# Optimization experiments

Measured on AMD Instinct MI355X. Metric: run time of the kernel, lower is better.

Reference implementation:

```python
import jax, jax.numpy as jnp
import numpy as np

N = 512
CZ = 128
CI = 128
LN_EPS = 1e-5


def _ln(x, w, b):
    m = jnp.mean(x, axis=-1, keepdims=True)
    v = jnp.mean(jnp.square(x - m), axis=-1, keepdims=True)
    return (x - m) * jax.lax.rsqrt(v + LN_EPS) * w + b


def setup_inputs() -> dict:
    key = jax.random.key(0)
    ks = jax.random.split(key, 8)
    s = 0.02
    return {
        "act": jax.random.normal(ks[0], (N, N, CZ), jnp.float32),
        "mask": jnp.ones((N, N), jnp.float32),
        "ln_in_w": jnp.ones((CZ,), jnp.float32),
        "ln_in_b": jnp.zeros((CZ,), jnp.float32),
        "proj_w": jax.random.normal(ks[1], (2 * CI, CZ), jnp.float32) * s,
        "proj_b": jnp.zeros((2 * CI,), jnp.float32),
        "gate_w": jax.random.normal(ks[2], (2 * CI, CI), jnp.float32) * s,
        "gate_b": jnp.zeros((2 * CI,), jnp.float32),
        "cn_w": jnp.ones((CI,), jnp.float32),
        "cn_b": jnp.zeros((CI,), jnp.float32),
        "outp_w": jax.random.normal(ks[3], (CZ, CI), jnp.float32) * s,
        "outp_b": jnp.zeros((CZ,), jnp.float32),
        "gl_w": jax.random.normal(ks[4], (CZ, CZ), jnp.float32) * s,
        "gl_b": jnp.zeros((CZ,), jnp.float32),
    }


def reference(act, mask, ln_in_w, ln_in_b, proj_w, proj_b, gate_w, gate_b,
              cn_w, cn_b, outp_w, outp_b, gl_w, gl_b):
    m = mask[..., None]                                    # [N,N,1]
    left = _ln(act, ln_in_w, ln_in_b)                      # [N,N,cz]
    proj = m * (left @ proj_w.T + proj_b)                  # [N,N,2ci]
    proj = proj * jax.nn.sigmoid(left @ gate_w.T + gate_b)
    ci = proj.shape[-1] // 2
    left_proj, right_proj = proj[..., :ci], proj[..., ci:]
    # triangle multiplication 'ikc,jkc->ijc' (outgoing edges)
    out = jnp.einsum('ikc,jkc->ijc', left_proj, right_proj)
    out = _ln(out, cn_w, cn_b)
    out = out @ outp_w.T + outp_b                          # [N,N,cz]
    out = out * jax.nn.sigmoid(left @ gl_w.T + gl_b)
    return out
```

## Files before the change

### kernel.cpp

```cpp
#include <hip/hip_runtime.h>
#include <stdint.h>

typedef unsigned short u16;
typedef uint32_t u32;
typedef _Float16 f16x8 __attribute__((ext_vector_type(8)));
typedef u16 u16x8 __attribute__((ext_vector_type(8)));
typedef float f32x4 __attribute__((ext_vector_type(4)));

#define MFMA(a,b,c) __builtin_amdgcn_mfma_f32_16x16x32_f16((a),(b),(c),0,0,0)

constexpr int SN = 512;
constexpr int CC = 128;
constexpr int PP = SN * SN;
constexpr float LNEPS = 1e-5f;
constexpr float LO_SCALE = 2048.0f;
constexpr float LO_INV   = 1.0f / 2048.0f;

__device__ __forceinline__ float bq(float f){
    u32 u = __builtin_bit_cast(u32, f);
    u += 0x7fffu + ((u >> 16) & 1u);
    return __builtin_bit_cast(float, u & 0xffff0000u);
}

__device__ __forceinline__ void split2(float x, u16& h, u16& l){
    _Float16 a = (_Float16)x;
    _Float16 b = (_Float16)((x - (float)a) * LO_SCALE);
    h = __builtin_bit_cast(u16, a);
    l = __builtin_bit_cast(u16, b);
}
__device__ __forceinline__ u16 f2h(float f){
    _Float16 h = (_Float16)f;
    return __builtin_bit_cast(u16, h);
}
__device__ __forceinline__ f16x8 ld_frag(const u16* p){
    return __builtin_bit_cast(f16x8, *(const u16x8*)p);
}
__device__ __forceinline__ float sigm(float x){ return 1.0f / (1.0f + __expf(-x)); }

__device__ __forceinline__ void load_w64s(const float* __restrict__ src,
                                          u16* dh, u16* dl, int tid){
    const int r = tid >> 2, q = tid & 3;
    const float4* s4 = (const float4*)(src + (size_t)r * CC + q * 32);
    __align__(16) u16 hbuf[32], lbuf[32];
    #pragma unroll
    for (int j = 0; j < 8; ++j){
        float4 v = s4[j];
        split2(bq(v.x), hbuf[j*4+0], lbuf[j*4+0]);
        split2(bq(v.y), hbuf[j*4+1], lbuf[j*4+1]);
        split2(bq(v.z), hbuf[j*4+2], lbuf[j*4+2]);
        split2(bq(v.w), hbuf[j*4+3], lbuf[j*4+3]);
    }
    uint4* ph = (uint4*)(dh + r * 136 + q * 32);
    uint4* pl = (uint4*)(dl + r * 136 + q * 32);
    #pragma unroll
    for (int w = 0; w < 4; ++w){
        ph[w] = ((const uint4*)hbuf)[w];
        pl[w] = ((const uint4*)lbuf)[w];
    }
}

__device__ __forceinline__ void ln_split(const float* __restrict__ act, int p0,
        const float* __restrict__ lnw, const float* __restrict__ lnb,
        u16* sLh, u16* sLl, int tid){
    const int pos = tid >> 2, q = tid & 3;
    const float4* a4 = (const float4*)(act + (size_t)(p0 + pos) * CC + q * 32);
    float4 av[8];
    float s = 0.f, s2 = 0.f;
    #pragma unroll
    for (int j = 0; j < 8; ++j){
        av[j] = a4[j];
        av[j].x = bq(av[j].x); av[j].y = bq(av[j].y);
        av[j].z = bq(av[j].z); av[j].w = bq(av[j].w);
        s  += av[j].x + av[j].y + av[j].z + av[j].w;
        s2 += av[j].x*av[j].x + av[j].y*av[j].y + av[j].z*av[j].z + av[j].w*av[j].w;
    }
    s  += __shfl_xor(s, 1);  s  += __shfl_xor(s, 2);
    s2 += __shfl_xor(s2, 1); s2 += __shfl_xor(s2, 2);
    const float mean = s * (1.f / CC);
    const float rstd = rsqrtf(s2 * (1.f / CC) - mean * mean + LNEPS);
    const float4* w4 = (const float4*)(lnw + q * 32);
    const float4* b4 = (const float4*)(lnb + q * 32);
    __align__(16) u16 hbuf[32], lbuf[32];
    #pragma unroll
    for (int j = 0; j < 8; ++j){
        float4 w = w4[j], b = b4[j];
        split2((av[j].x - mean) * rstd * bq(w.x) + bq(b.x), hbuf[j*4+0], lbuf[j*4+0]);
        split2((av[j].y - mean) * rstd * bq(w.y) + bq(b.y), hbuf[j*4+1], lbuf[j*4+1]);
        split2((av[j].z - mean) * rstd * bq(w.z) + bq(b.z), hbuf[j*4+2], lbuf[j*4+2]);
        split2((av[j].w - mean) * rstd * bq(w.w) + bq(b.w), hbuf[j*4+3], lbuf[j*4+3]);
    }
    uint4* ph = (uint4*)(sLh + pos * 136 + q * 32);
    uint4* pl = (uint4*)(sLl + pos * 136 + q * 32);
    #pragma unroll
    for (int w = 0; w < 4; ++w){
        ph[w] = ((const uint4*)hbuf)[w];
        pl[w] = ((const uint4*)lbuf)[w];
    }
}

__device__ __forceinline__ void gemm64s(const u16* sLh, const u16* sLl,
        const u16* sWh, const u16* sWl, int wave, int lq, int lr, f32x4* res){
    f32x4 ah[4], al[4];
    #pragma unroll
    for (int t = 0; t < 4; ++t){ ah[t] = f32x4{0,0,0,0}; al[t] = f32x4{0,0,0,0}; }
    #pragma unroll
    for (int kk = 0; kk < 4; ++kk){
        const int ao = (wave*16 + lr) * 136 + kk * 32 + lq * 8;
        const f16x8 a_h = ld_frag(sLh + ao);
        const f16x8 a_l = ld_frag(sLl + ao);
        #pragma unroll
        for (int t = 0; t < 4; ++t){
            const int bo = (t*16 + lr) * 136 + kk * 32 + lq * 8;
            const f16x8 b_h = ld_frag(sWh + bo);
            const f16x8 b_l = ld_frag(sWl + bo);
            ah[t] = MFMA(a_h, b_h, ah[t]);
            al[t] = MFMA(a_h, b_l, al[t]);
            al[t] = MFMA(a_l, b_h, al[t]);
        }
    }
    #pragma unroll
    for (int t = 0; t < 4; ++t) res[t] = ah[t] + al[t] * LO_INV;
}

__global__ __launch_bounds__(256) void k1_ln_proj(
        const float* __restrict__ act,  const float* __restrict__ mask,
        const float* __restrict__ lnw,  const float* __restrict__ lnb,
        const float* __restrict__ projw,const float* __restrict__ projb,
        const float* __restrict__ gatew,const float* __restrict__ gateb,
        u16* __restrict__ lph, u16* __restrict__ lpl,
        u16* __restrict__ rph, u16* __restrict__ rpl)
{
    __shared__ __align__(16) u16 sLh[64*136], sLl[64*136];
    __shared__ __align__(16) u16 sW[2*64*136];
    u16* sWh = sW;
    u16* sWl = sW + 64*136;

    const int tid  = threadIdx.x;
    const int p0   = blockIdx.x * 64;
    const int irow = p0 >> 9;
    const int k0   = p0 & 511;

    ln_split(act, p0, lnw, lnb, sLh, sLl, tid);

    const int wave = tid >> 6, lane = tid & 63, lq = lane >> 4, lr = lane & 15;
    const float4 mv = *(const float4*)(mask + p0 + wave*16 + lq*4);
    const float mr[4] = {bq(mv.x), bq(mv.y), bq(mv.z), bq(mv.w)};

    #pragma unroll 1
    for (int gh = 0; gh < 4; ++gh){
        const int g = gh >> 1, h = gh & 1;
        const int cb = g * 128 + h * 64;

        __syncthreads();
        load_w64s(gatew + (size_t)cb * CC, sWh, sWl, tid);
        __syncthreads();
        f32x4 gres[4]; gemm64s(sLh, sLl, sWh, sWl, wave, lq, lr, gres);
        __syncthreads();
        load_w64s(projw + (size_t)cb * CC, sWh, sWl, tid);
        __syncthreads();
        f32x4 pres[4]; gemm64s(sLh, sLl, sWh, sWl, wave, lq, lr, pres);
        __syncthreads();

        u16* sTh = sW;
        u16* sTl = sW + 64*72;
        const int pos0 = wave * 16 + lq * 4;
        #pragma unroll
        for (int t = 0; t < 4; ++t){
            const int col = t * 16 + lr;
            const float qb = bq(gateb[cb + col]);
            const float pb = bq(projb[cb + col]);
            __align__(8) u16 th[4], tl[4];
            #pragma unroll
            for (int r = 0; r < 4; ++r){
                const float v = mr[r] * (pres[t][r] + pb) * sigm(gres[t][r] + qb);
                split2(v, th[r], tl[r]);
            }
            *(uint2*)(sTh + col * 72 + pos0) = *(const uint2*)th;
            *(uint2*)(sTl + col * 72 + pos0) = *(const uint2*)tl;
        }
        __syncthreads();

        {
            const int cl = tid >> 2, q = tid & 3;
            const size_t off = (size_t)(h*64 + cl) * PP + (size_t)irow * SN + k0 + q * 16;
            u16* dh = (g ? rph : lph) + off;
            const u16* sh = sTh + cl * 72 + q * 16;
            ((uint4*)dh)[0] = ((const uint4*)sh)[0];
            ((uint4*)dh)[1] = ((const uint4*)sh)[1];
            u16* lob = g ? rpl : lpl;
            if (lob){
                u16* dl = lob + off;
                const u16* sl = sTl + cl * 72 + q * 16;
                ((uint4*)dl)[0] = ((const uint4*)sl)[0];
                ((uint4*)dl)[1] = ((const uint4*)sl)[1];
            }
        }
    }
}

template<int RPS, int OT16>
__global__ __launch_bounds__(256) void k2_einsum(
        const u16* __restrict__ lph, const u16* __restrict__ lpl,
        const u16* __restrict__ rph, const u16* __restrict__ rpl,
        void* __restrict__ outTv)
{
    __shared__ __align__(16) u16 sAh[128*72], sAl[128*72], sBh[128*72];
    __shared__ __align__(16) u16 sBl[RPS ? 128*72 : 8];
    const int tid = threadIdx.x;
    const int bid = blockIdx.x;
    const int swz = (bid & 7) * 256 + (bid >> 3);
    const int c   = swz >> 4;
    const int i0  = ((swz >> 2) & 3) * 128;
    const int j0  = (swz & 3) * 128;
    const size_t aoff = (size_t)c * PP + (size_t)i0 * SN;
    const size_t boff = (size_t)c * PP + (size_t)j0 * SN;
    const int wave = tid >> 6, lane = tid & 63, lq = lane >> 4, lr = lane & 15;
    const int wi = (wave & 1) * 64, wj = (wave >> 1) * 64;
    const int row = tid >> 1, half = tid & 1;
    const size_t goff = (size_t)row * SN + half * 32;

    f32x4 acch[4][4], accl[4][4];
    #pragma unroll
    for (int m = 0; m < 4; ++m)
        #pragma unroll
        for (int n = 0; n < 4; ++n){ acch[m][n] = f32x4{0,0,0,0}; accl[m][n] = f32x4{0,0,0,0}; }

    for (int k0 = 0; k0 < SN; k0 += 64){
        const uint4* gah = (const uint4*)(lph + aoff + goff + k0);
        const uint4* gal = (const uint4*)(lpl + aoff + goff + k0);
        const uint4* gbh = (const uint4*)(rph + boff + goff + k0);
        uint4 Ah0 = gah[0], Ah1 = gah[1], Ah2 = gah[2], Ah3 = gah[3];
        uint4 Al0 = gal[0], Al1 = gal[1], Al2 = gal[2], Al3 = gal[3];
        uint4 Bh0 = gbh[0], Bh1 = gbh[1], Bh2 = gbh[2], Bh3 = gbh[3];
        uint4 Bl0, Bl1, Bl2, Bl3;
        if (RPS){
            const uint4* gbl = (const uint4*)(rpl + boff + goff + k0);
            Bl0 = gbl[0]; Bl1 = gbl[1]; Bl2 = gbl[2]; Bl3 = gbl[3];
        }
        __syncthreads();
        uint4* dah = (uint4*)(sAh + row * 72 + half * 32);
        uint4* dal = (uint4*)(sAl + row * 72 + half * 32);
        uint4* dbh = (uint4*)(sBh + row * 72 + half * 32);
        dah[0] = Ah0; dah[1] = Ah1; dah[2] = Ah2; dah[3] = Ah3;
        dal[0] = Al0; dal[1] = Al1; dal[2] = Al2; dal[3] = Al3;
        dbh[0] = Bh0; dbh[1] = Bh1; dbh[2] = Bh2; dbh[3] = Bh3;
        if (RPS){
            uint4* dbl = (uint4*)(sBl + row * 72 + half * 32);
            dbl[0] = Bl0; dbl[1] = Bl1; dbl[2] = Bl2; dbl[3] = Bl3;
        }
        __syncthreads();
        #pragma unroll
        for (int kk = 0; kk < 64; kk += 32){
            f16x8 ahf[4], alf[4], bhf[4], blf[RPS ? 4 : 1];
            #pragma unroll
            for (int m = 0; m < 4; ++m){
                const int ro = (wi + m*16 + lr) * 72 + kk + lq * 8;
                ahf[m] = ld_frag(sAh + ro);
                alf[m] = ld_frag(sAl + ro);
            }
            #pragma unroll
            for (int n = 0; n < 4; ++n){
                const int ro = (wj + n*16 + lr) * 72 + kk + lq * 8;
                bhf[n] = ld_frag(sBh + ro);
                if (RPS) blf[n] = ld_frag(sBl + ro);
            }
            #pragma unroll
            for (int m = 0; m < 4; ++m)
                #pragma unroll
                for (int n = 0; n < 4; ++n){
                    acch[m][n] = MFMA(ahf[m], bhf[n], acch[m][n]);
                    accl[m][n] = MFMA(alf[m], bhf[n], accl[m][n]);
                    if (RPS) accl[m][n] = MFMA(ahf[m], blf[n], accl[m][n]);
                }
        }
    }
    #pragma unroll
    for (int m = 0; m < 4; ++m){
        const int ir = i0 + wi + m * 16 + lq * 4;
        #pragma unroll
        for (int n = 0; n < 4; ++n){
            const int jc = j0 + wj + n * 16 + lr;
            #pragma unroll
            for (int r = 0; r < 4; ++r){
                const float v = acch[m][n][r] + accl[m][n][r] * LO_INV;
                if (OT16)
                    ((u16*)outTv)[(size_t)c * PP + (size_t)(ir + r) * SN + jc] = f2h(v);
                else
                    ((float*)outTv)[(size_t)c * PP + (size_t)(ir + r) * SN + jc] = v;
            }
        }
    }
}

template<int OT16>
__global__ __launch_bounds__(256) void k3_out(
        const float* __restrict__ act,  const void* __restrict__ outTv,
        const float* __restrict__ lnw,  const float* __restrict__ lnb,
        const float* __restrict__ glw,  const float* __restrict__ glb,
        const float* __restrict__ cnw,  const float* __restrict__ cnb,
        const float* __restrict__ outpw,const float* __restrict__ outpb,
        float* __restrict__ io)
{
    __shared__ __align__(16) char smem[36864 + 34816];
    __shared__ float sRed[64 * 8];
    __shared__ float sStat[64 * 2];
    char* regA = smem;
    char* regB = smem + 36864;

    const int tid  = threadIdx.x;
    const int p0   = blockIdx.x * 64;
    const int irow = p0 >> 9;
    const int j0   = p0 & 511;
    const int wave = tid >> 6, lane = tid & 63, lq = lane >> 4, lr = lane & 15;

    u16* sLh = (u16*)regA; u16* sLl = sLh + 64*136;
    u16* sGh = (u16*)regB; u16* sGl = sGh + 64*136;
    ln_split(act, p0, lnw, lnb, sLh, sLl, tid);
    f32x4 gate[8];
    #pragma unroll 1
    for (int ch = 0; ch < 2; ++ch){
        __syncthreads();
        load_w64s(glw + (size_t)(ch * 64) * CC, sGh, sGl, tid);
        __syncthreads();
        f32x4 res[4]; gemm64s(sLh, sLl, sGh, sGl, wave, lq, lr, res);
        #pragma unroll
        for (int t = 0; t < 4; ++t){
            const float gb = bq(glb[ch*64 + t*16 + lr]);
            f32x4 gv;
            #pragma unroll
            for (int r = 0; r < 4; ++r) gv[r] = sigm(res[t][r] + gb);
            gate[ch*4 + t] = gv;
        }
    }
    __syncthreads();

    float* sRaw = (float*)regA;
    {
        const int cc = tid >> 1, hf = tid & 1;
        if (OT16){
            const uint4* g4 = (const uint4*)((const u16*)outTv
                    + (size_t)cc * PP + (size_t)irow * SN + j0 + hf * 32);
            uint4 v[4];
            #pragma unroll
            for (int j = 0; j < 4; ++j) v[j] = g4[j];
            float* d = sRaw + cc * 72 + hf * 32;
            #pragma unroll
            for (int j = 0; j < 4; ++j){
                u16x8 hh = __builtin_bit_cast(u16x8, v[j]);
                #pragma unroll
                for (int e = 0; e < 8; ++e)
                    d[j*8+e] = (float)__builtin_bit_cast(_Float16, hh[e]);
            }
        } else {
            const float4* g4 = (const float4*)((const float*)outTv
                    + (size_t)cc * PP + (size_t)irow * SN + j0 + hf * 32);
            float4 v[8];
            #pragma unroll
            for (int j = 0; j < 8; ++j) v[j] = g4[j];
            float4* d = (float4*)(sRaw + cc * 72 + hf * 32);
            #pragma unroll
            for (int j = 0; j < 8; ++j) d[j] = v[j];
        }
    }
    __syncthreads();

    const int jj = tid & 63, cq = tid >> 6;
    {
        float s = 0.f, s2 = 0.f;
        #pragma unroll
        for (int t = 0; t < 32; ++t){
            float x = sRaw[(cq*32 + t) * 72 + jj];
            s += x; s2 += x * x;
        }
        sRed[jj*8 + cq] = s; sRed[jj*8 + 4 + cq] = s2;
    }
    __syncthreads();
    if (tid < 64){
        float s  = sRed[tid*8+0] + sRed[tid*8+1] + sRed[tid*8+2] + sRed[tid*8+3];
        float s2 = sRed[tid*8+4] + sRed[tid*8+5] + sRed[tid*8+6] + sRed[tid*8+7];
        float mean = s * (1.f / CC);
        sStat[tid*2+0] = mean;
        sStat[tid*2+1] = rsqrtf(s2 * (1.f / CC) - mean * mean + LNEPS);
    }
    __syncthreads();
    u16* sNh = (u16*)regB; u16* sNl = sNh + 64*136;
    {
        const float mean = sStat[jj*2+0], rstd = sStat[jj*2+1];
        __align__(16) u16 nh[32], nl[32];
        #pragma unroll
        for (int t = 0; t < 32; ++t){
            const int ch = cq * 32 + t;
            const float x = (sRaw[ch * 72 + jj] - mean) * rstd * bq(cnw[ch]) + bq(cnb[ch]);
            split2(x, nh[t], nl[t]);
        }
        uint4* dh = (uint4*)(sNh + jj*136 + cq*32);
        uint4* dl = (uint4*)(sNl + jj*136 + cq*32);
        #pragma unroll
        for (int w = 0; w < 4; ++w){
            dh[w] = ((const uint4*)nh)[w];
            dl[w] = ((const uint4*)nl)[w];
        }
    }
    u16* sOh = (u16*)regA; u16* sOl = sOh + 64*136;
    #pragma unroll 1
    for (int hf = 0; hf < 2; ++hf){
        __syncthreads();
        load_w64s(outpw + (size_t)(hf * 64) * CC, sOh, sOl, tid);
        __syncthreads();
        f32x4 res[4]; gemm64s(sNh, sNl, sOh, sOl, cq, lq, lr, res);
        #pragma unroll
        for (int t = 0; t < 4; ++t){
            const int col = hf*64 + t*16 + lr;
            const float ob = bq(outpb[col]);
            #pragma unroll
            for (int r = 0; r < 4; ++r){
                const int pos = p0 + cq*16 + lq*4 + r;
                io[(size_t)pos * CC + col] = (res[t][r] + ob) * gate[hf*4 + t][r];
            }
        }
    }
}

extern "C" void kernel_launch(void* const* d_in, const int* in_sizes, int n_in,
                              void* d_out, int out_size, void* d_ws, size_t ws_size,
                              hipStream_t stream)
{
    const float* act   = (const float*)d_in[0];
    const float* mask  = (const float*)d_in[1];
    const float* lnw   = (const float*)d_in[2];
    const float* lnb   = (const float*)d_in[3];
    const float* projw = (const float*)d_in[4];
    const float* projb = (const float*)d_in[5];
    const float* gatew = (const float*)d_in[6];
    const float* gateb = (const float*)d_in[7];
    const float* cnw   = (const float*)d_in[8];
    const float* cnb   = (const float*)d_in[9];
    const float* outpw = (const float*)d_in[10];
    const float* outpb = (const float*)d_in[11];
    const float* glw   = (const float*)d_in[12];
    const float* glb   = (const float*)d_in[13];

    const size_t E    = (size_t)PP * CC;
    const size_t MB64 = E * sizeof(u16);
    u16* lph = (u16*)d_ws;
    u16* lpl = lph + E;
    u16* rph = lpl + E;

    if (ws_size >= 6 * MB64){
        u16*   rpl  = rph + E;
        float* outT = (float*)(rpl + E);
        k1_ln_proj<<<PP / 64, 256, 0, stream>>>(act, mask, lnw, lnb, projw, projb,
                                                gatew, gateb, lph, lpl, rph, rpl);
        k2_einsum<1,0><<<2048, 256, 0, stream>>>(lph, lpl, rph, rpl, outT);
        k3_out<0><<<PP / 64, 256, 0, stream>>>(act, outT, lnw, lnb, glw, glb,
                                               cnw, cnb, outpw, outpb, (float*)d_out);
    } else if (ws_size >= 5 * MB64){
        u16* rpl  = rph + E;
        u16* outT = rpl + E;
        k1_ln_proj<<<PP / 64, 256, 0, stream>>>(act, mask, lnw, lnb, projw, projb,
                                                gatew, gateb, lph, lpl, rph, rpl);
        k2_einsum<1,1><<<2048, 256, 0, stream>>>(lph, lpl, rph, rpl, outT);
        k3_out<1><<<PP / 64, 256, 0, stream>>>(act, outT, lnw, lnb, glw, glb,
                                               cnw, cnb, outpw, outpb, (float*)d_out);
    } else {
        u16* outT = rph + E;
        k1_ln_proj<<<PP / 64, 256, 0, stream>>>(act, mask, lnw, lnb, projw, projb,
                                                gatew, gateb, lph, lpl, rph, nullptr);
        k2_einsum<0,1><<<2048, 256, 0, stream>>>(lph, lpl, rph, nullptr, outT);
        k3_out<1><<<PP / 64, 256, 0, stream>>>(act, outT, lnw, lnb, glw, glb,
                                               cnw, cnb, outpw, outpb, (float*)d_out);
    }
}
```

Baseline: 885.8 us.

## Pre-split weights once and keep LN activations in register fragments

Adds a small prologue kernel that converts all four weight matrices to fp16 hi/lo pairs once per call, so k1 and k3 copy pre-split weights into LDS instead of re-quantizing them in every block. The LayerNorm output is now built directly into per-lane MFMA A-fragments held in registers rather than staged through shared memory. This cuts the LDS footprint of k1 and k3 (with launch bounds raised to target three blocks per CU) and removes some barriers. The cost is higher register pressure, one extra launch, and workspace use that can push the large-buffer path down to a smaller variant when workspace is tight.

```diff
diff --git a/kernel.cpp b/kernel.cpp
--- a/kernel.cpp
+++ b/kernel.cpp
@@ -16,6 +16,12 @@
 constexpr float LO_SCALE = 2048.0f;
 constexpr float LO_INV   = 1.0f / 2048.0f;
 
+constexpr int GATE_OFF = 0;
+constexpr int PROJ_OFF = 32768;
+constexpr int GL_OFF   = 65536;
+constexpr int OUTP_OFF = 81920;
+constexpr int WTOT     = 98304;
+
 __device__ __forceinline__ float bq(float f){
     u32 u = __builtin_bit_cast(u32, f);
     u += 0x7fffu + ((u >> 16) & 1u);
@@ -36,6 +42,41 @@
     return __builtin_bit_cast(f16x8, *(const u16x8*)p);
 }
 __device__ __forceinline__ float sigm(float x){ return 1.0f / (1.0f + __expf(-x)); }
+
+__global__ __launch_bounds__(256) void k0_wsplit(
+        const float* __restrict__ gatew, const float* __restrict__ projw,
+        const float* __restrict__ glw,   const float* __restrict__ outpw,
+        u16* __restrict__ wh, u16* __restrict__ wl)
+{
+    const int e = (blockIdx.x * 256 + threadIdx.x) * 4;
+    const float* src; int o;
+    if      (e < PROJ_OFF){ src = gatew; o = e; }
+    else if (e < GL_OFF)  { src = projw; o = e - PROJ_OFF; }
+    else if (e < OUTP_OFF){ src = glw;   o = e - GL_OFF; }
+    else                  { src = outpw; o = e - OUTP_OFF; }
+    const float4 v = *(const float4*)(src + o);
+    __align__(8) u16 h[4], l[4];
+    split2(bq(v.x), h[0], l[0]);
+    split2(bq(v.y), h[1], l[1]);
+    split2(bq(v.z), h[2], l[2]);
+    split2(bq(v.w), h[3], l[3]);
+    *(uint2*)(wh + e) = *(const uint2*)h;
+    *(uint2*)(wl + e) = *(const uint2*)l;
+}
+
+__device__ __forceinline__ void stage_pre(const u16* __restrict__ sh_,
+        const u16* __restrict__ sl_, u16* dh, u16* dl, int tid){
+    const int r = tid >> 2, q = tid & 3;
+    const uint4* s1 = (const uint4*)(sh_ + r * CC + q * 32);
+    const uint4* s2 = (const uint4*)(sl_ + r * CC + q * 32);
+    uint4* d1 = (uint4*)(dh + r * 136 + q * 32);
+    uint4* d2 = (uint4*)(dl + r * 136 + q * 32);
+    #pragma unroll
+    for (int w = 0; w < 4; ++w){
+        d1[w] = s1[w];
+        d2[w] = s2[w];
+    }
+}
 
 __device__ __forceinline__ void load_w64s(const float* __restrict__ src,
                                           u16* dh, u16* dl, int tid){
@@ -59,55 +100,56 @@
     }
 }
 
-__device__ __forceinline__ void ln_split(const float* __restrict__ act, int p0,
+__device__ __forceinline__ void ln_frag(const float* __restrict__ act, int p0,
         const float* __restrict__ lnw, const float* __restrict__ lnb,
-        u16* sLh, u16* sLl, int tid){
-    const int pos = tid >> 2, q = tid & 3;
-    const float4* a4 = (const float4*)(act + (size_t)(p0 + pos) * CC + q * 32);
+        int wave, int lq, int lr, f16x8* fh, f16x8* fl)
+{
+    const float* base = act + (size_t)(p0 + wave*16 + lr) * CC + lq * 8;
     float4 av[8];
     float s = 0.f, s2 = 0.f;
     #pragma unroll
-    for (int j = 0; j < 8; ++j){
-        av[j] = a4[j];
-        av[j].x = bq(av[j].x); av[j].y = bq(av[j].y);
-        av[j].z = bq(av[j].z); av[j].w = bq(av[j].w);
-        s  += av[j].x + av[j].y + av[j].z + av[j].w;
-        s2 += av[j].x*av[j].x + av[j].y*av[j].y + av[j].z*av[j].z + av[j].w*av[j].w;
-    }
-    s  += __shfl_xor(s, 1);  s  += __shfl_xor(s, 2);
-    s2 += __shfl_xor(s2, 1); s2 += __shfl_xor(s2, 2);
+    for (int kk = 0; kk < 4; ++kk){
+        #pragma unroll
+        for (int j = 0; j < 2; ++j){
+            float4 v = *(const float4*)(base + kk*32 + j*4);
+            v.x = bq(v.x); v.y = bq(v.y); v.z = bq(v.z); v.w = bq(v.w);
+            av[kk*2+j] = v;
+            s  += v.x + v.y + v.z + v.w;
+            s2 += v.x*v.x + v.y*v.y + v.z*v.z + v.w*v.w;
+        }
+    }
+    s  += __shfl_xor(s, 16);  s  += __shfl_xor(s, 32);
+    s2 += __shfl_xor(s2, 16); s2 += __shfl_xor(s2, 32);
     const float mean = s * (1.f / CC);
     const float rstd = rsqrtf(s2 * (1.f / CC) - mean * mean + LNEPS);
-    const float4* w4 = (const float4*)(lnw + q * 32);
-    const float4* b4 = (const float4*)(lnb + q * 32);
-    __align__(16) u16 hbuf[32], lbuf[32];
-    #pragma unroll
-    for (int j = 0; j < 8; ++j){
-        float4 w = w4[j], b = b4[j];
-        split2((av[j].x - mean) * rstd * bq(w.x) + bq(b.x), hbuf[j*4+0], lbuf[j*4+0]);
-        split2((av[j].y - mean) * rstd * bq(w.y) + bq(b.y), hbuf[j*4+1], lbuf[j*4+1]);
-        split2((av[j].z - mean) * rstd * bq(w.z) + bq(b.z), hbuf[j*4+2], lbuf[j*4+2]);
-        split2((av[j].w - mean) * rstd * bq(w.w) + bq(b.w), hbuf[j*4+3], lbuf[j*4+3]);
-    }
-    uint4* ph = (uint4*)(sLh + pos * 136 + q * 32);
-    uint4* pl = (uint4*)(sLl + pos * 136 + q * 32);
-    #pragma unroll
-    for (int w = 0; w < 4; ++w){
-        ph[w] = ((const uint4*)hbuf)[w];
-        pl[w] = ((const uint4*)lbuf)[w];
-    }
-}
-
-__device__ __forceinline__ void gemm64s(const u16* sLh, const u16* sLl,
-        const u16* sWh, const u16* sWl, int wave, int lq, int lr, f32x4* res){
+    #pragma unroll
+    for (int kk = 0; kk < 4; ++kk){
+        __align__(16) u16 h[8], l[8];
+        #pragma unroll
+        for (int j = 0; j < 2; ++j){
+            const float4 v = av[kk*2+j];
+            const float4 w = *(const float4*)(lnw + lq*8 + kk*32 + j*4);
+            const float4 b = *(const float4*)(lnb + lq*8 + kk*32 + j*4);
+            split2((v.x-mean)*rstd*bq(w.x)+bq(b.x), h[j*4+0], l[j*4+0]);
+            split2((v.y-mean)*rstd*bq(w.y)+bq(b.y), h[j*4+1], l[j*4+1]);
+            split2((v.z-mean)*rstd*bq(w.z)+bq(b.z), h[j*4+2], l[j*4+2]);
+            split2((v.w-mean)*rstd*bq(w.w)+bq(b.w), h[j*4+3], l[j*4+3]);
+        }
+        fh[kk] = __builtin_bit_cast(f16x8, *(const u16x8*)h);
+        fl[kk] = __builtin_bit_cast(f16x8, *(const u16x8*)l);
+    }
+}
+
+__device__ __forceinline__ void gemm64r(const f16x8* fh, const f16x8* fl,
+        const u16* __restrict__ sWh, const u16* __restrict__ sWl,
+        int lq, int lr, f32x4* res)
+{
     f32x4 ah[4], al[4];
     #pragma unroll
     for (int t = 0; t < 4; ++t){ ah[t] = f32x4{0,0,0,0}; al[t] = f32x4{0,0,0,0}; }
     #pragma unroll
     for (int kk = 0; kk < 4; ++kk){
-        const int ao = (wave*16 + lr) * 136 + kk * 32 + lq * 8;
-        const f16x8 a_h = ld_frag(sLh + ao);
-        const f16x8 a_l = ld_frag(sLl + ao);
+        const f16x8 a_h = fh[kk], a_l = fl[kk];
         #pragma unroll
         for (int t = 0; t < 4; ++t){
             const int bo = (t*16 + lr) * 136 + kk * 32 + lq * 8;
@@ -122,27 +164,29 @@
     for (int t = 0; t < 4; ++t) res[t] = ah[t] + al[t] * LO_INV;
 }
 
-__global__ __launch_bounds__(256) void k1_ln_proj(
+__global__ __launch_bounds__(256, 3) void k1_ln_proj(
         const float* __restrict__ act,  const float* __restrict__ mask,
         const float* __restrict__ lnw,  const float* __restrict__ lnb,
         const float* __restrict__ projw,const float* __restrict__ projb,
         const float* __restrict__ gatew,const float* __restrict__ gateb,
+        const u16* __restrict__ wph,    const u16* __restrict__ wpl,
         u16* __restrict__ lph, u16* __restrict__ lpl,
         u16* __restrict__ rph, u16* __restrict__ rpl)
 {
-    __shared__ __align__(16) u16 sLh[64*136], sLl[64*136];
     __shared__ __align__(16) u16 sW[2*64*136];
-    u16* sWh = sW;
-    u16* sWl = sW + 64*136;
+    __shared__ __align__(16) u16 sT[2*64*72];
+    u16* sWh = sW;  u16* sWl = sW + 64*136;
+    u16* sTh = sT;  u16* sTl = sT + 64*72;
 
     const int tid  = threadIdx.x;
     const int p0   = blockIdx.x * 64;
     const int irow = p0 >> 9;
     const int k0   = p0 & 511;
-
-    ln_split(act, p0, lnw, lnb, sLh, sLl, tid);
-
     const int wave = tid >> 6, lane = tid & 63, lq = lane >> 4, lr = lane & 15;
+
+    f16x8 fh[4], fl[4];
+    ln_frag(act, p0, lnw, lnb, wave, lq, lr, fh, fl);
+
     const float4 mv = *(const float4*)(mask + p0 + wave*16 + lq*4);
     const float mr[4] = {bq(mv.x), bq(mv.y), bq(mv.z), bq(mv.w)};
 
@@ -152,17 +196,16 @@
         const int cb = g * 128 + h * 64;
 
         __syncthreads();
-        load_w64s(gatew + (size_t)cb * CC, sWh, sWl, tid);
-        __syncthreads();
-        f32x4 gres[4]; gemm64s(sLh, sLl, sWh, sWl, wave, lq, lr, gres);
-        __syncthreads();
-        load_w64s(projw + (size_t)cb * CC, sWh, sWl, tid);
-        __syncthreads();
-        f32x4 pres[4]; gemm64s(sLh, sLl, sWh, sWl, wave, lq, lr, pres);
-        __syncthreads();
-
-        u16* sTh = sW;
-        u16* sTl = sW + 64*72;
+        if (wph) stage_pre(wph + GATE_OFF + cb*CC, wpl + GATE_OFF + cb*CC, sWh, sWl, tid);
+        else     load_w64s(gatew + (size_t)cb * CC, sWh, sWl, tid);
+        __syncthreads();
+        f32x4 gres[4]; gemm64r(fh, fl, sWh, sWl, lq, lr, gres);
+        __syncthreads();
+        if (wph) stage_pre(wph + PROJ_OFF + cb*CC, wpl + PROJ_OFF + cb*CC, sWh, sWl, tid);
+        else     load_w64s(projw + (size_t)cb * CC, sWh, sWl, tid);
+        __syncthreads();
+        f32x4 pres[4]; gemm64r(fh, fl, sWh, sWl, lq, lr, pres);
+
         const int pos0 = wave * 16 + lq * 4;
         #pragma unroll
         for (int t = 0; t < 4; ++t){
@@ -184,15 +227,15 @@
             const int cl = tid >> 2, q = tid & 3;
             const size_t off = (size_t)(h*64 + cl) * PP + (size_t)irow * SN + k0 + q * 16;
             u16* dh = (g ? rph : lph) + off;
-            const u16* sh = sTh + cl * 72 + q * 16;
-            ((uint4*)dh)[0] = ((const uint4*)sh)[0];
-            ((uint4*)dh)[1] = ((const uint4*)sh)[1];
+            const u16* shp = sTh + cl * 72 + q * 16;
+            ((uint4*)dh)[0] = ((const uint4*)shp)[0];
+            ((uint4*)dh)[1] = ((const uint4*)shp)[1];
             u16* lob = g ? rpl : lpl;
             if (lob){
                 u16* dl = lob + off;
-                const u16* sl = sTl + cl * 72 + q * 16;
-                ((uint4*)dl)[0] = ((const uint4*)sl)[0];
-                ((uint4*)dl)[1] = ((const uint4*)sl)[1];
+                const u16* slp = sTl + cl * 72 + q * 16;
+                ((uint4*)dl)[0] = ((const uint4*)slp)[0];
+                ((uint4*)dl)[1] = ((const uint4*)slp)[1];
             }
         }
     }
@@ -293,19 +336,18 @@
 }
 
 template<int OT16>
-__global__ __launch_bounds__(256) void k3_out(
+__global__ __launch_bounds__(256, 3) void k3_out(
         const float* __restrict__ act,  const void* __restrict__ outTv,
         const float* __restrict__ lnw,  const float* __restrict__ lnb,
         const float* __restrict__ glw,  const float* __restrict__ glb,
         const float* __restrict__ cnw,  const float* __restrict__ cnb,
         const float* __restrict__ outpw,const float* __restrict__ outpb,
+        const u16* __restrict__ wph,    const u16* __restrict__ wpl,
         float* __restrict__ io)
 {
-    __shared__ __align__(16) char smem[36864 + 34816];
+    __shared__ __align__(16) char smem[36864];
     __shared__ float sRed[64 * 8];
     __shared__ float sStat[64 * 2];
-    char* regA = smem;
-    char* regB = smem + 36864;
 
     const int tid  = threadIdx.x;
     const int p0   = blockIdx.x * 64;
@@ -313,16 +355,17 @@
     const int j0   = p0 & 511;
     const int wave = tid >> 6, lane = tid & 63, lq = lane >> 4, lr = lane & 15;
 
-    u16* sLh = (u16*)regA; u16* sLl = sLh + 64*136;
-    u16* sGh = (u16*)regB; u16* sGl = sGh + 64*136;
-    ln_split(act, p0, lnw, lnb, sLh, sLl, tid);
+    u16* sGh = (u16*)smem; u16* sGl = sGh + 64*136;
+    f16x8 fh[4], fl[4];
+    ln_frag(act, p0, lnw, lnb, wave, lq, lr, fh, fl);
     f32x4 gate[8];
     #pragma unroll 1
     for (int ch = 0; ch < 2; ++ch){
         __syncthreads();
-        load_w64s(glw + (size_t)(ch * 64) * CC, sGh, sGl, tid);
-        __syncthreads();
-        f32x4 res[4]; gemm64s(sLh, sLl, sGh, sGl, wave, lq, lr, res);
+        if (wph) stage_pre(wph + GL_OFF + ch*64*CC, wpl + GL_OFF + ch*64*CC, sGh, sGl, tid);
+        else     load_w64s(glw + (size_t)(ch * 64) * CC, sGh, sGl, tid);
+        __syncthreads();
+        f32x4 res[4]; gemm64r(fh, fl, sGh, sGl, lq, lr, res);
         #pragma unroll
         for (int t = 0; t < 4; ++t){
             const float gb = bq(glb[ch*64 + t*16 + lr]);
@@ -334,16 +377,16 @@
     }
     __syncthreads();
 
-    float* sRaw = (float*)regA;
+    float* sRaw = (float*)smem;
     {
-        const int cc = tid >> 1, hf = tid & 1;
+        const int cc = tid >> 1, hfj = tid & 1;
         if (OT16){
             const uint4* g4 = (const uint4*)((const u16*)outTv
-                    + (size_t)cc * PP + (size_t)irow * SN + j0 + hf * 32);
+                    + (size_t)cc * PP + (size_t)irow * SN + j0 + hfj * 32);
             uint4 v[4];
             #pragma unroll
             for (int j = 0; j < 4; ++j) v[j] = g4[j];
-            float* d = sRaw + cc * 72 + hf * 32;
+            float* d = sRaw + cc * 72 + hfj * 32;
             #pragma unroll
             for (int j = 0; j < 4; ++j){
                 u16x8 hh = __builtin_bit_cast(u16x8, v[j]);
@@ -353,26 +396,26 @@
             }
         } else {
             const float4* g4 = (const float4*)((const float*)outTv
-                    + (size_t)cc * PP + (size_t)irow * SN + j0 + hf * 32);
+                    + (size_t)cc * PP + (size_t)irow * SN + j0 + hfj * 32);
             float4 v[8];
             #pragma unroll
             for (int j = 0; j < 8; ++j) v[j] = g4[j];
-            float4* d = (float4*)(sRaw + cc * 72 + hf * 32);
+            float4* d = (float4*)(sRaw + cc * 72 + hfj * 32);
             #pragma unroll
             for (int j = 0; j < 8; ++j) d[j] = v[j];
         }
     }
     __syncthreads();
 
-    const int jj = tid & 63, cq = tid >> 6;
+    const int jj = tid & 63;
     {
         float s = 0.f, s2 = 0.f;
         #pragma unroll
         for (int t = 0; t < 32; ++t){
-            float x = sRaw[(cq*32 + t) * 72 + jj];
+            float x = sRaw[(wave*32 + t) * 72 + jj];
             s += x; s2 += x * x;
         }
-        sRed[jj*8 + cq] = s; sRed[jj*8 + 4 + cq] = s2;
+        sRed[jj*8 + wave] = s; sRed[jj*8 + 4 + wave] = s2;
     }
     __syncthreads();
     if (tid < 64){
@@ -383,41 +426,48 @@
         sStat[tid*2+1] = rsqrtf(s2 * (1.f / CC) - mean * mean + LNEPS);
     }
     __syncthreads();
-    u16* sNh = (u16*)regB; u16* sNl = sNh + 64*136;
+
+    f16x8 nh[4], nl2[4];
     {
-        const float mean = sStat[jj*2+0], rstd = sStat[jj*2+1];
-        __align__(16) u16 nh[32], nl[32];
-        #pragma unroll
-        for (int t = 0; t < 32; ++t){
-            const int ch = cq * 32 + t;
-            const float x = (sRaw[ch * 72 + jj] - mean) * rstd * bq(cnw[ch]) + bq(cnb[ch]);
-            split2(x, nh[t], nl[t]);
-        }
-        uint4* dh = (uint4*)(sNh + jj*136 + cq*32);
-        uint4* dl = (uint4*)(sNl + jj*136 + cq*32);
-        #pragma unroll
-        for (int w = 0; w < 4; ++w){
-            dh[w] = ((const uint4*)nh)[w];
-            dl[w] = ((const uint4*)nl)[w];
-        }
-    }
-    u16* sOh = (u16*)regA; u16* sOl = sOh + 64*136;
+        const int row = wave * 16 + lr;
+        const float mean = sStat[row*2+0], rstd = sStat[row*2+1];
+        #pragma unroll
+        for (int kk = 0; kk < 4; ++kk){
+            __align__(16) u16 h[8], l[8];
+            #pragma unroll
+            for (int j = 0; j < 2; ++j){
+                const int ch = kk*32 + lq*8 + j*4;
+                const float4 w = *(const float4*)(cnw + ch);
+                const float4 b = *(const float4*)(cnb + ch);
+                split2((sRaw[(ch+0)*72+row]-mean)*rstd*bq(w.x)+bq(b.x), h[j*4+0], l[j*4+0]);
+                split2((sRaw[(ch+1)*72+row]-mean)*rstd*bq(w.y)+bq(b.y), h[j*4+1], l[j*4+1]);
+                split2((sRaw[(ch+2)*72+row]-mean)*rstd*bq(w.z)+bq(b.z), h[j*4+2], l[j*4+2]);
+                split2((sRaw[(ch+3)*72+row]-mean)*rstd*bq(w.w)+bq(b.w), h[j*4+3], l[j*4+3]);
+            }
+            nh[kk]  = __builtin_bit_cast(f16x8, *(const u16x8*)h);
+            nl2[kk] = __builtin_bit_cast(f16x8, *(const u16x8*)l);
+        }
+    }
+    __syncthreads();
+
+    u16* sOh = (u16*)smem; u16* sOl = sOh + 64*136;
     #pragma unroll 1
     for (int hf = 0; hf < 2; ++hf){
-        __syncthreads();
-        load_w64s(outpw + (size_t)(hf * 64) * CC, sOh, sOl, tid);
-        __syncthreads();
-        f32x4 res[4]; gemm64s(sNh, sNl, sOh, sOl, cq, lq, lr, res);
+        if (wph) stage_pre(wph + OUTP_OFF + hf*64*CC, wpl + OUTP_OFF + hf*64*CC, sOh, sOl, tid);
+        else     load_w64s(outpw + (size_t)(hf * 64) * CC, sOh, sOl, tid);
+        __syncthreads();
+        f32x4 res[4]; gemm64r(nh, nl2, sOh, sOl, lq, lr, res);
         #pragma unroll
         for (int t = 0; t < 4; ++t){
             const int col = hf*64 + t*16 + lr;
             const float ob = bq(outpb[col]);
             #pragma unroll
             for (int r = 0; r < 4; ++r){
-                const int pos = p0 + cq*16 + lq*4 + r;
+                const int pos = p0 + wave*16 + lq*4 + r;
                 io[(size_t)pos * CC + col] = (res[t][r] + ob) * gate[hf*4 + t][r];
             }
         }
+        __syncthreads();
     }
 }
 
@@ -442,32 +492,44 @@
 
     const size_t E    = (size_t)PP * CC;
     const size_t MB64 = E * sizeof(u16);
-    u16* lph = (u16*)d_ws;
+    const size_t WB   = (size_t)WTOT * 2 * sizeof(u16);
+
+    u16* wph = nullptr; u16* wpl = nullptr;
+    u16* base = (u16*)d_ws; size_t avail = ws_size;
+    if (ws_size >= 4 * MB64 + WB){
+        wph = (u16*)d_ws; wpl = wph + WTOT; base = wpl + WTOT; avail = ws_size - WB;
+    }
+    u16* lph = base;
     u16* lpl = lph + E;
     u16* rph = lpl + E;
 
-    if (ws_size >= 6 * MB64){
+    if (wph) k0_wsplit<<<WTOT / 1024, 256, 0, stream>>>(gatew, projw, glw, outpw, wph, wpl);
+
+    if (avail >= 6 * MB64){
         u16*   rpl  = rph + E;
         float* outT = (float*)(rpl + E);
         k1_ln_proj<<<PP / 64, 256, 0, stream>>>(act, mask, lnw, lnb, projw, projb,
-                                                gatew, gateb, lph, lpl, rph, rpl);
+                                                gatew, gateb, wph, wpl, lph, lpl, rph, rpl);
         k2_einsum<1,0><<<2048, 256, 0, stream>>>(lph, lpl, rph, rpl, outT);
         k3_out<0><<<PP / 64, 256, 0, stream>>>(act, outT, lnw, lnb, glw, glb,
-                                               cnw, cnb, outpw, outpb, (float*)d_out);
-    } else if (ws_size >= 5 * MB64){
+                                               cnw, cnb, outpw, outpb, wph, wpl,
+                                               (float*)d_out);
+    } else if (avail >= 5 * MB64){
         u16* rpl  = rph + E;
         u16* outT = rpl + E;
         k1_ln_proj<<<PP / 64, 256, 0, stream>>>(act, mask, lnw, lnb, projw, projb,
-                                                gatew, gateb, lph, lpl, rph, rpl);
+                                                gatew, gateb, wph, wpl, lph, lpl, rph, rpl);
         k2_einsum<1,1><<<2048, 256, 0, stream>>>(lph, lpl, rph, rpl, outT);
         k3_out<1><<<PP / 64, 256, 0, stream>>>(act, outT, lnw, lnb, glw, glb,
-                                               cnw, cnb, outpw, outpb, (float*)d_out);
+                                               cnw, cnb, outpw, outpb, wph, wpl,
+                                               (float*)d_out);
     } else {
         u16* outT = rph + E;
         k1_ln_proj<<<PP / 64, 256, 0, stream>>>(act, mask, lnw, lnb, projw, projb,
-                                                gatew, gateb, lph, lpl, rph, nullptr);
+                                                gatew, gateb, wph, wpl, lph, lpl, rph, nullptr);
         k2_einsum<0,1><<<2048, 256, 0, stream>>>(lph, lpl, rph, nullptr, outT);
         k3_out<1><<<PP / 64, 256, 0, stream>>>(act, outT, lnw, lnb, glw, glb,
-                                               cnw, cnb, outpw, outpb, (float*)d_out);
-    }
-}
+                                               cnw, cnb, outpw, outpb, wph, wpl,
+                                               (float*)d_out);
+    }
+}
```

Result: faster. 751.6 us (-15.2%).
